# Performance work log

Measured on AMD Instinct MI355X. Metric: run time of the kernel, lower is better.

## Reference

```python
import jax, jax.numpy as jnp
import numpy as np

N, K = 8192, 133
N_LAYERS = 6
HID = 64
# mmpose RealNVP coupling masks: [0,1],[1,0] repeated 3 times
MASK = jnp.array([[0.0, 1.0], [1.0, 0.0]] * 3, dtype=jnp.float32)  # [6,2]


def _mlp(x, w1, b1, w2, b2, w3, b3):
    # x: [P,2] -> [P,2]; LeakyReLU slope 0.01 (torch default)
    h = jax.nn.leaky_relu(x @ w1.T + b1, 0.01)
    h = jax.nn.leaky_relu(h @ w2.T + b2, 0.01)
    return h @ w3.T + b3


def _flow_log_prob(x, s_w1, s_b1, s_w2, s_b2, s_w3, s_b3,
                   t_w1, t_b1, t_w2, t_b2, t_w3, t_b3):
    # RealNVP backward pass: x -> z, accumulating log-det Jacobian
    z = x
    log_det = jnp.zeros(x.shape[0], x.dtype)
    for i in reversed(range(N_LAYERS)):
        m = MASK[i]
        z_ = m * z
        s = jnp.tanh(_mlp(z_, s_w1[i], s_b1[i], s_w2[i], s_b2[i], s_w3[i], s_b3[i])) * (1.0 - m)
        t = _mlp(z_, t_w1[i], t_b1[i], t_w2[i], t_b2[i], t_w3[i], t_b3[i]) * (1.0 - m)
        z = (1.0 - m) * (z - t) * jnp.exp(-s) + z_
        log_det = log_det - s.sum(axis=1)
    # standard 2D normal prior log-prob
    prior_lp = -0.5 * jnp.sum(z * z, axis=1) - jnp.log(2.0 * jnp.pi)
    return prior_lp + log_det


def setup_inputs() -> dict:
    key = jax.random.key(0)
    ks = jax.random.split(key, 16)
    inp = {
        'pred': jax.random.normal(ks[0], (N, K, 4), dtype=jnp.float32),
        'target': jax.random.normal(ks[1], (N, K, 2), dtype=jnp.float32),
        'target_weight': jax.random.uniform(ks[2], (N, K), dtype=jnp.float32),
    }
    dims = [(HID, 2), (HID,), (HID, HID), (HID,), (2, HID), (2,)]
    names = ['w1', 'b1', 'w2', 'b2', 'w3', 'b3']
    kidx = 3
    for pfx in ('s', 't'):
        for nm, d in zip(names, dims):
            inp[f'{pfx}_{nm}'] = 0.1 * jax.random.normal(ks[kidx], (N_LAYERS,) + d, dtype=jnp.float32)
            kidx += 1
    return inp


def reference(pred, target, target_weight,
              s_w1, s_b1, s_w2, s_b2, s_w3, s_b3,
              t_w1, t_b1, t_w2, t_b2, t_w3, t_b3):
    miu = pred[:, :, :2]
    sigma = jnp.sqrt(jnp.abs(pred[:, :, 2:4]))  # sigmoid=False
    error = (miu - target) / (sigma + 1e-9)  # [N,K,2]
    log_phi = _flow_log_prob(error.reshape(-1, 2),
                             s_w1, s_b1, s_w2, s_b2, s_w3, s_b3,
                             t_w1, t_b1, t_w2, t_b2, t_w3, t_b3)
    log_phi = log_phi.reshape(pred.shape[0], pred.shape[1], 1)
    log_sigma = jnp.log(sigma)
    nf_loss = log_sigma - log_phi  # [N,K,2]
    # residual=True, q_distribution='laplace'
    loss_q = jnp.log(sigma * 2.0) + jnp.abs(error)
    loss = nf_loss + loss_q
    loss = loss * target_weight[:, :, None]  # use_target_weight=True
    loss = loss / pred.shape[0]  # size_average=True: divide by len(loss)=N
    return loss.sum()
```

## Files before the change

kernel.cpp:

```cpp
#include <hip/hip_runtime.h>

typedef _Float16 hfrag_t __attribute__((ext_vector_type(8)));
typedef _Float16 h2_t    __attribute__((ext_vector_type(2)));
typedef __attribute__((ext_vector_type(4))) float    f4_t;
typedef __attribute__((ext_vector_type(4))) unsigned u4_t;

#define LOG_2PI   1.8378770664093453f
#define TWO_LOG2  1.3862943611198906f
#define T_TILES   8
#define BLOCK     256
#define PTS_BLK   512
#define ZCLAMP    30000.0f

__device__ __forceinline__ unsigned pkh(float a, float b) {
  return __builtin_bit_cast(unsigned, __builtin_amdgcn_cvt_pkrtz(a, b));
}
__device__ __forceinline__ unsigned pk_fma_h(unsigned a, unsigned b, unsigned c) {
  unsigned d;
  asm("v_pk_fma_f16 %0, %1, %2, %3" : "=v"(d) : "v"(a), "v"(b), "v"(c));
  return d;
}
__device__ __forceinline__ unsigned pk_leaky_h(unsigned h, unsigned k01) {
  unsigned t, r;
  asm("v_pk_mul_f16 %0, %1, %2" : "=v"(t) : "v"(h), "v"(k01));
  asm("v_pk_max_f16 %0, %1, %2" : "=v"(r) : "v"(h), "v"(t));
  return r;
}
__device__ __forceinline__ float dot2h(unsigned a, unsigned b, float c) {
  return __builtin_amdgcn_fdot2(__builtin_bit_cast(h2_t, a), __builtin_bit_cast(h2_t, b), c, false);
}

__device__ __forceinline__ void stage_layer(u4_t* afr, const float* sW2, const float* tW2,
                                            int layer, int tid) {
  #pragma unroll
  for (int it = 0; it < 4; ++it) {
    int idx = tid + it * BLOCK;
    int l = idx & 63, f = (idx >> 6) & 7, m = (idx >> 9) & 1;
    int n = f & 3, q = f >> 2;
    int row = 16 * n + (l & 15), kb = 32 * q + 8 * (l >> 4);
    const float* src = (m ? tW2 : sW2) + layer * 4096 + row * 64 + kb;
    float4 a = *(const float4*)src;
    float4 b = *(const float4*)(src + 4);
    afr[(m * 8 + f) * 64 + l] =
        (u4_t){pkh(a.x, a.y), pkh(a.z, a.w), pkh(b.x, b.y), pkh(b.z, b.w)};
  }
}

__global__ __launch_bounds__(BLOCK)
void ihll_kernel(
    const float* __restrict__ pred, const float* __restrict__ targ, const float* __restrict__ twp,
    const float* __restrict__ sW1, const float* __restrict__ sB1, const float* __restrict__ sW2,
    const float* __restrict__ sB2, const float* __restrict__ sW3, const float* __restrict__ sB3,
    const float* __restrict__ tW1, const float* __restrict__ tB1, const float* __restrict__ tW2,
    const float* __restrict__ tB2, const float* __restrict__ tW3, const float* __restrict__ tB3,
    float* __restrict__ out, int M) {
  __shared__ u4_t     afr[2 * 8 * 64];
  __shared__ float4   zld[PTS_BLK];
  __shared__ float    pre0v[PTS_BLK];
  __shared__ unsigned c1h[6][2][32];
  __shared__ unsigned b1h[6][2][32];
  __shared__ unsigned w3h[6][2][4][8];
  __shared__ float    b2s[6][2][64];
  __shared__ float    wsum[4];

  const int tid  = threadIdx.x;
  const int lane = tid & 63, wave = tid >> 6;
  const int pr   = lane & 15, g = lane >> 4;
  const int pbase = blockIdx.x * PTS_BLK;
  const unsigned k01h = pkh(0.01f, 0.01f);

  for (int idx = tid; idx < 384; idx += BLOCK) {
    int i = idx >> 6, r = idx & 63, m = r >> 5, jp = r & 31;
    int jo = i & 1, jm = jo ^ 1;
    const float* w1 = m ? tW1 : sW1;  const float* b1 = m ? tB1 : sB1;
    c1h[i][m][jp] = pkh(w1[i * 128 + 4 * jp + jm], w1[i * 128 + 4 * jp + 2 + jm]);
    b1h[i][m][jp] = pkh(b1[i * 64 + 2 * jp], b1[i * 64 + 2 * jp + 1]);
  }
  for (int idx = tid; idx < 384; idx += BLOCK) {
    int i = idx >> 6, r = idx & 63, m = r >> 5, c = r & 31;
    int gg = c >> 3, c2 = c & 7, n = c2 >> 1, jj = c2 & 1;
    int jo = i & 1;
    const float* w3 = m ? tW3 : sW3;
    int row = 16 * n + 4 * gg + 2 * jj;
    w3h[i][m][gg][c2] = pkh(w3[i * 128 + jo * 64 + row], w3[i * 128 + jo * 64 + row + 1]);
  }
  for (int idx = tid; idx < 768; idx += BLOCK) {
    int i = idx >> 7, r = idx & 127, m = r >> 6, j = r & 63;
    const float* b2 = m ? tB2 : sB2;
    b2s[i][m][j] = b2[i * 64 + j];
  }
  #pragma unroll
  for (int it = 0; it < 2; ++it) {
    int idx = tid + it * BLOCK;
    int P = pbase + idx;
    float4 zs = make_float4(0.f, 0.f, 0.f, 0.f);
    if (P < M) {
      float4 p4 = ((const float4*)pred)[P];
      float2 t2 = ((const float2*)targ)[P];
      float s0 = sqrtf(fabsf(p4.z)), s1 = sqrtf(fabsf(p4.w));
      zs.x = (p4.x - t2.x) / (s0 + 1e-9f);
      zs.y = (p4.y - t2.y) / (s1 + 1e-9f);
    }
    zld[idx] = zs;
  }
  stage_layer(afr, sW2, tW2, 5, tid);
  __syncthreads();

  const int wbase = wave * (T_TILES * 16);
  const float* zldf = (const float*)zld;

  #pragma unroll 1
  for (int li = 0; li < 6; ++li) {
    const int i = 5 - li;
    const int jo = i & 1;
    const bool upd0 = (jo == 0);
    const float b3s = sB3[i * 2 + jo];
    const float b3t = tB3[i * 2 + jo];

    #pragma unroll
    for (int m = 0; m < 2; ++m) {
      u4_t af[8];
      #pragma unroll
      for (int f = 0; f < 8; ++f)
        af[f] = afr[(m * 8 + f) * 64 + lane];
      unsigned c1q[8], b1q[8];
      *(u4_t*)&c1q[0] = *(const u4_t*)&c1h[i][m][4 * g];
      *(u4_t*)&c1q[4] = *(const u4_t*)&c1h[i][m][16 + 4 * g];
      *(u4_t*)&b1q[0] = *(const u4_t*)&b1h[i][m][4 * g];
      *(u4_t*)&b1q[4] = *(const u4_t*)&b1h[i][m][16 + 4 * g];
      unsigned w3q[8];
      *(u4_t*)&w3q[0] = *(const u4_t*)&w3h[i][m][g][0];
      *(u4_t*)&w3q[4] = *(const u4_t*)&w3h[i][m][g][4];
      f4_t b2q[4];
      #pragma unroll
      for (int n = 0; n < 4; ++n)
        b2q[n] = *(const f4_t*)&b2s[i][m][n * 16 + 4 * g];

      #pragma unroll 1
      for (int t = 0; t < T_TILES; ++t) {
        const int widx = wbase + t * 16 + pr;
        float4 zv;
        float zin;
        if (m == 1) { zv = zld[widx]; zin = upd0 ? zv.y : zv.x; }
        else        { zin = zldf[4 * widx + (upd0 ? 1 : 0)]; }
        float zc = fmaxf(fminf(zin, ZCLAMP), -ZCLAMP);
        const unsigned zz = pkh(zc, zc);

        f4_t acc[4];
        #pragma unroll
        for (int q = 0; q < 2; ++q) {
          unsigned hh[4];
          #pragma unroll
          for (int e = 0; e < 4; ++e)
            hh[e] = pk_leaky_h(pk_fma_h(c1q[q * 4 + e], zz, b1q[q * 4 + e]), k01h);
          hfrag_t B = __builtin_bit_cast(hfrag_t, (u4_t){hh[0], hh[1], hh[2], hh[3]});
          #pragma unroll
          for (int n = 0; n < 4; ++n) {
            f4_t c = (q == 0) ? b2q[n] : acc[n];
            acc[n] = __builtin_amdgcn_mfma_f32_16x16x32_f16(
                __builtin_bit_cast(hfrag_t, af[q * 4 + n]), B, c, 0, 0, 0);
          }
        }
        float pa = 0.f;
        #pragma unroll
        for (int n = 0; n < 4; ++n) {
          unsigned x01 = pk_leaky_h(pkh(acc[n][0], acc[n][1]), k01h);
          unsigned x23 = pk_leaky_h(pkh(acc[n][2], acc[n][3]), k01h);
          pa = dot2h(x01, w3q[2 * n], pa);
          pa = dot2h(x23, w3q[2 * n + 1], pa);
        }
        pa += __shfl_xor(pa, 16);
        pa += __shfl_xor(pa, 32);

        if (m == 0) {
          if (g == 0) pre0v[widx] = pa;
        } else {
          float p0  = pre0v[widx];
          float sv  = 1.f - 2.f / (__expf(2.f * (p0 + b3s)) + 1.f);
          float tv  = pa + b3t;
          float zo  = upd0 ? zv.x : zv.y;
          float zn  = (zo - tv) * __expf(-sv);
          if (upd0) zv.x = zn; else zv.y = zn;
          zv.z -= sv;
          if (g == 0) zld[widx] = zv;
        }
      }
    }
    __syncthreads();
    if (li < 5) {
      stage_layer(afr, sW2, tW2, i - 1, tid);
      __syncthreads();
    }
  }

  float csum = 0.f;
  #pragma unroll
  for (int it = 0; it < 2; ++it) {
    int idx = tid + it * BLOCK;
    int P = pbase + idx;
    if (P < M) {
      float4 p4 = ((const float4*)pred)[P];
      float2 t2 = ((const float2*)targ)[P];
      float w   = twp[P];
      float s0 = sqrtf(fabsf(p4.z)), s1 = sqrtf(fabsf(p4.w));
      float e0 = (p4.x - t2.x) / (s0 + 1e-9f);
      float e1 = (p4.y - t2.y) / (s1 + 1e-9f);
      float bs = 2.f * (logf(s0) + logf(s1)) + TWO_LOG2 + fabsf(e0) + fabsf(e1);
      float4 zv = zld[idx];
      float prior = -0.5f * (zv.x * zv.x + zv.y * zv.y) - LOG_2PI;
      float lphi  = prior + zv.z;
      csum += (bs - 2.f * lphi) * w;
    }
  }
  #pragma unroll
  for (int off = 1; off <= 32; off <<= 1)
    csum += __shfl_xor(csum, off);
  if (lane == 0) wsum[wave] = csum;
  __syncthreads();
  if (tid == 0) {
    float tot = wsum[0] + wsum[1] + wsum[2] + wsum[3];
    atomicAdd(out, tot * (1.0f / 8192.0f));
  }
}

extern "C" void kernel_launch(void* const* d_in, const int* in_sizes, int n_in,
                              void* d_out, int out_size, void* d_ws, size_t ws_size,
                              hipStream_t stream) {
  const float* pred = (const float*)d_in[0];
  const float* targ = (const float*)d_in[1];
  const float* twp  = (const float*)d_in[2];
  const float* sW1 = (const float*)d_in[3];  const float* sB1 = (const float*)d_in[4];
  const float* sW2 = (const float*)d_in[5];  const float* sB2 = (const float*)d_in[6];
  const float* sW3 = (const float*)d_in[7];  const float* sB3 = (const float*)d_in[8];
  const float* tW1 = (const float*)d_in[9];  const float* tB1 = (const float*)d_in[10];
  const float* tW2 = (const float*)d_in[11]; const float* tB2 = (const float*)d_in[12];
  const float* tW3 = (const float*)d_in[13]; const float* tB3 = (const float*)d_in[14];

  const int M = in_sizes[2];
  const int blocks = (M + PTS_BLK - 1) / PTS_BLK;

  hipMemsetAsync(d_out, 0, sizeof(float), stream);
  hipLaunchKernelGGL(ihll_kernel, dim3(blocks), dim3(BLOCK), 0, stream,
                     pred, targ, twp, sW1, sB1, sW2, sB2, sW3, sB3,
                     tW1, tB1, tW2, tB2, tW3, tB3, (float*)d_out, M);
}
```

Before: 232.0 us.

## Process four point tiles per iteration to interleave MFMA chains

The inner tile loop now handles four 16-point tiles at once, giving four independent MFMA accumulator chains and four independent layer-1/epilogue streams so MFMA latency can be hidden by ILP. The s-network partial sums are reduced across lanes as packed fp16 pairs to cut shuffle count, and the kernel is hinted to run at 2 waves per EU. In exchange it raises register pressure and reduces the s-branch pre-activation sum to fp16 precision before the tanh.

```diff
diff --git a/kernel.cpp b/kernel.cpp
--- a/kernel.cpp
+++ b/kernel.cpp
@@ -18,6 +18,11 @@
 __device__ __forceinline__ unsigned pk_fma_h(unsigned a, unsigned b, unsigned c) {
   unsigned d;
   asm("v_pk_fma_f16 %0, %1, %2, %3" : "=v"(d) : "v"(a), "v"(b), "v"(c));
+  return d;
+}
+__device__ __forceinline__ unsigned pk_add_h(unsigned a, unsigned b) {
+  unsigned d;
+  asm("v_pk_add_f16 %0, %1, %2" : "=v"(d) : "v"(a), "v"(b));
   return d;
 }
 __device__ __forceinline__ unsigned pk_leaky_h(unsigned h, unsigned k01) {
@@ -47,6 +52,7 @@
 }
 
 __global__ __launch_bounds__(BLOCK)
+__attribute__((amdgpu_waves_per_eu(2)))
 void ihll_kernel(
     const float* __restrict__ pred, const float* __restrict__ targ, const float* __restrict__ twp,
     const float* __restrict__ sW1, const float* __restrict__ sB1, const float* __restrict__ sW2,
@@ -107,7 +113,6 @@
   __syncthreads();
 
   const int wbase = wave * (T_TILES * 16);
-  const float* zldf = (const float*)zld;
 
   #pragma unroll 1
   for (int li = 0; li < 6; ++li) {
@@ -137,52 +142,113 @@
         b2q[n] = *(const f4_t*)&b2s[i][m][n * 16 + 4 * g];
 
       #pragma unroll 1
-      for (int t = 0; t < T_TILES; ++t) {
-        const int widx = wbase + t * 16 + pr;
-        float4 zv;
-        float zin;
-        if (m == 1) { zv = zld[widx]; zin = upd0 ? zv.y : zv.x; }
-        else        { zin = zldf[4 * widx + (upd0 ? 1 : 0)]; }
-        float zc = fmaxf(fminf(zin, ZCLAMP), -ZCLAMP);
-        const unsigned zz = pkh(zc, zc);
-
-        f4_t acc[4];
+      for (int tt = 0; tt < T_TILES / 4; ++tt) {
+        const int w0 = wbase + (4 * tt) * 16 + pr;
+        float4 zv0 = zld[w0];
+        float4 zv1 = zld[w0 + 16];
+        float4 zv2 = zld[w0 + 32];
+        float4 zv3 = zld[w0 + 48];
+        float zi0 = upd0 ? zv0.y : zv0.x;
+        float zi1 = upd0 ? zv1.y : zv1.x;
+        float zi2 = upd0 ? zv2.y : zv2.x;
+        float zi3 = upd0 ? zv3.y : zv3.x;
+        zi0 = fmaxf(fminf(zi0, ZCLAMP), -ZCLAMP);
+        zi1 = fmaxf(fminf(zi1, ZCLAMP), -ZCLAMP);
+        zi2 = fmaxf(fminf(zi2, ZCLAMP), -ZCLAMP);
+        zi3 = fmaxf(fminf(zi3, ZCLAMP), -ZCLAMP);
+        const unsigned zz0 = pkh(zi0, zi0), zz1 = pkh(zi1, zi1);
+        const unsigned zz2 = pkh(zi2, zi2), zz3 = pkh(zi3, zi3);
+
+        f4_t acc0[4], acc1[4], acc2[4], acc3[4];
         #pragma unroll
         for (int q = 0; q < 2; ++q) {
-          unsigned hh[4];
+          unsigned h0[4], h1v[4], h2v[4], h3[4];
           #pragma unroll
-          for (int e = 0; e < 4; ++e)
-            hh[e] = pk_leaky_h(pk_fma_h(c1q[q * 4 + e], zz, b1q[q * 4 + e]), k01h);
-          hfrag_t B = __builtin_bit_cast(hfrag_t, (u4_t){hh[0], hh[1], hh[2], hh[3]});
+          for (int e = 0; e < 4; ++e) {
+            h0[e]  = pk_leaky_h(pk_fma_h(c1q[q * 4 + e], zz0, b1q[q * 4 + e]), k01h);
+            h1v[e] = pk_leaky_h(pk_fma_h(c1q[q * 4 + e], zz1, b1q[q * 4 + e]), k01h);
+            h2v[e] = pk_leaky_h(pk_fma_h(c1q[q * 4 + e], zz2, b1q[q * 4 + e]), k01h);
+            h3[e]  = pk_leaky_h(pk_fma_h(c1q[q * 4 + e], zz3, b1q[q * 4 + e]), k01h);
+          }
+          hfrag_t B0 = __builtin_bit_cast(hfrag_t, (u4_t){h0[0], h0[1], h0[2], h0[3]});
+          hfrag_t B1 = __builtin_bit_cast(hfrag_t, (u4_t){h1v[0], h1v[1], h1v[2], h1v[3]});
+          hfrag_t B2 = __builtin_bit_cast(hfrag_t, (u4_t){h2v[0], h2v[1], h2v[2], h2v[3]});
+          hfrag_t B3 = __builtin_bit_cast(hfrag_t, (u4_t){h3[0], h3[1], h3[2], h3[3]});
           #pragma unroll
           for (int n = 0; n < 4; ++n) {
-            f4_t c = (q == 0) ? b2q[n] : acc[n];
-            acc[n] = __builtin_amdgcn_mfma_f32_16x16x32_f16(
-                __builtin_bit_cast(hfrag_t, af[q * 4 + n]), B, c, 0, 0, 0);
+            hfrag_t A = __builtin_bit_cast(hfrag_t, af[q * 4 + n]);
+            acc0[n] = __builtin_amdgcn_mfma_f32_16x16x32_f16(A, B0, (q == 0) ? b2q[n] : acc0[n], 0, 0, 0);
+            acc1[n] = __builtin_amdgcn_mfma_f32_16x16x32_f16(A, B1, (q == 0) ? b2q[n] : acc1[n], 0, 0, 0);
+            acc2[n] = __builtin_amdgcn_mfma_f32_16x16x32_f16(A, B2, (q == 0) ? b2q[n] : acc2[n], 0, 0, 0);
+            acc3[n] = __builtin_amdgcn_mfma_f32_16x16x32_f16(A, B3, (q == 0) ? b2q[n] : acc3[n], 0, 0, 0);
           }
         }
-        float pa = 0.f;
+        float p0a = 0.f, p0b = 0.f, p1a = 0.f, p1b = 0.f;
+        float p2a = 0.f, p2b = 0.f, p3a = 0.f, p3b = 0.f;
         #pragma unroll
         for (int n = 0; n < 4; ++n) {
-          unsigned x01 = pk_leaky_h(pkh(acc[n][0], acc[n][1]), k01h);
-          unsigned x23 = pk_leaky_h(pkh(acc[n][2], acc[n][3]), k01h);
-          pa = dot2h(x01, w3q[2 * n], pa);
-          pa = dot2h(x23, w3q[2 * n + 1], pa);
+          unsigned a01 = pk_leaky_h(pkh(acc0[n][0], acc0[n][1]), k01h);
+          unsigned a23 = pk_leaky_h(pkh(acc0[n][2], acc0[n][3]), k01h);
+          unsigned b01 = pk_leaky_h(pkh(acc1[n][0], acc1[n][1]), k01h);
+          unsigned b23 = pk_leaky_h(pkh(acc1[n][2], acc1[n][3]), k01h);
+          unsigned c01 = pk_leaky_h(pkh(acc2[n][0], acc2[n][1]), k01h);
+          unsigned c23 = pk_leaky_h(pkh(acc2[n][2], acc2[n][3]), k01h);
+          unsigned d01 = pk_leaky_h(pkh(acc3[n][0], acc3[n][1]), k01h);
+          unsigned d23 = pk_leaky_h(pkh(acc3[n][2], acc3[n][3]), k01h);
+          if (n < 2) {
+            p0a = dot2h(a01, w3q[2 * n], p0a);  p0a = dot2h(a23, w3q[2 * n + 1], p0a);
+            p1a = dot2h(b01, w3q[2 * n], p1a);  p1a = dot2h(b23, w3q[2 * n + 1], p1a);
+            p2a = dot2h(c01, w3q[2 * n], p2a);  p2a = dot2h(c23, w3q[2 * n + 1], p2a);
+            p3a = dot2h(d01, w3q[2 * n], p3a);  p3a = dot2h(d23, w3q[2 * n + 1], p3a);
+          } else {
+            p0b = dot2h(a01, w3q[2 * n], p0b);  p0b = dot2h(a23, w3q[2 * n + 1], p0b);
+            p1b = dot2h(b01, w3q[2 * n], p1b);  p1b = dot2h(b23, w3q[2 * n + 1], p1b);
+            p2b = dot2h(c01, w3q[2 * n], p2b);  p2b = dot2h(c23, w3q[2 * n + 1], p2b);
+            p3b = dot2h(d01, w3q[2 * n], p3b);  p3b = dot2h(d23, w3q[2 * n + 1], p3b);
+          }
         }
-        pa += __shfl_xor(pa, 16);
-        pa += __shfl_xor(pa, 32);
+        float pt0 = p0a + p0b, pt1 = p1a + p1b, pt2 = p2a + p2b, pt3 = p3a + p3b;
 
         if (m == 0) {
-          if (g == 0) pre0v[widx] = pa;
+          unsigned r01 = pkh(pt0, pt1), r23 = pkh(pt2, pt3);
+          r01 = pk_add_h(r01, __shfl_xor(r01, 16));
+          r23 = pk_add_h(r23, __shfl_xor(r23, 16));
+          r01 = pk_add_h(r01, __shfl_xor(r01, 32));
+          r23 = pk_add_h(r23, __shfl_xor(r23, 32));
+          if (g == 0) {
+            h2_t v01 = __builtin_bit_cast(h2_t, r01);
+            h2_t v23 = __builtin_bit_cast(h2_t, r23);
+            pre0v[w0]      = (float)v01[0];
+            pre0v[w0 + 16] = (float)v01[1];
+            pre0v[w0 + 32] = (float)v23[0];
+            pre0v[w0 + 48] = (float)v23[1];
+          }
         } else {
-          float p0  = pre0v[widx];
-          float sv  = 1.f - 2.f / (__expf(2.f * (p0 + b3s)) + 1.f);
-          float tv  = pa + b3t;
-          float zo  = upd0 ? zv.x : zv.y;
-          float zn  = (zo - tv) * __expf(-sv);
-          if (upd0) zv.x = zn; else zv.y = zn;
-          zv.z -= sv;
-          if (g == 0) zld[widx] = zv;
+          pt0 += __shfl_xor(pt0, 16);  pt0 += __shfl_xor(pt0, 32);
+          pt1 += __shfl_xor(pt1, 16);  pt1 += __shfl_xor(pt1, 32);
+          pt2 += __shfl_xor(pt2, 16);  pt2 += __shfl_xor(pt2, 32);
+          pt3 += __shfl_xor(pt3, 16);  pt3 += __shfl_xor(pt3, 32);
+          float s0v = 1.f - 2.f / (__expf(2.f * (pre0v[w0]      + b3s)) + 1.f);
+          float s1v = 1.f - 2.f / (__expf(2.f * (pre0v[w0 + 16] + b3s)) + 1.f);
+          float s2v = 1.f - 2.f / (__expf(2.f * (pre0v[w0 + 32] + b3s)) + 1.f);
+          float s3v = 1.f - 2.f / (__expf(2.f * (pre0v[w0 + 48] + b3s)) + 1.f);
+          float zo0 = upd0 ? zv0.x : zv0.y;
+          float zo1 = upd0 ? zv1.x : zv1.y;
+          float zo2 = upd0 ? zv2.x : zv2.y;
+          float zo3 = upd0 ? zv3.x : zv3.y;
+          float zn0 = (zo0 - (pt0 + b3t)) * __expf(-s0v);
+          float zn1 = (zo1 - (pt1 + b3t)) * __expf(-s1v);
+          float zn2 = (zo2 - (pt2 + b3t)) * __expf(-s2v);
+          float zn3 = (zo3 - (pt3 + b3t)) * __expf(-s3v);
+          if (upd0) { zv0.x = zn0; zv1.x = zn1; zv2.x = zn2; zv3.x = zn3; }
+          else      { zv0.y = zn0; zv1.y = zn1; zv2.y = zn2; zv3.y = zn3; }
+          zv0.z -= s0v;  zv1.z -= s1v;  zv2.z -= s2v;  zv3.z -= s3v;
+          if (g == 0) {
+            zld[w0]      = zv0;
+            zld[w0 + 16] = zv1;
+            zld[w0 + 32] = zv2;
+            zld[w0 + 48] = zv3;
+          }
         }
       }
     }
```

After: 224.7 us, median of 2. 3.1% less time.

## Keep per-point flow state in registers and unroll tile loop with smaller blocks

Applied to the files above, without the earlier changes.

Each point's flow state (z0, z1, log-det and the s-branch pre-activation) now lives in per-thread registers instead of shared-memory arrays. This removes LDS reads and writes from every tile of every layer. The tile loop is fully unrolled, points per block are halved, and a waves-per-EU hint is added to trade register pressure for occupancy. Because all four lane groups now hold the same point, the epilogue counts each point four times. The final scale is divided by four more to compensate, and the log/sqrt epilogue work is repeated redundantly per lane group.

```diff
diff --git a/kernel.cpp b/kernel.cpp
--- a/kernel.cpp
+++ b/kernel.cpp
@@ -7,9 +7,9 @@
 
 #define LOG_2PI   1.8378770664093453f
 #define TWO_LOG2  1.3862943611198906f
-#define T_TILES   8
+#define T_TILES   4
 #define BLOCK     256
-#define PTS_BLK   512
+#define PTS_BLK   256
 #define ZCLAMP    30000.0f
 
 __device__ __forceinline__ unsigned pkh(float a, float b) {
@@ -47,6 +47,7 @@
 }
 
 __global__ __launch_bounds__(BLOCK)
+__attribute__((amdgpu_waves_per_eu(4)))
 void ihll_kernel(
     const float* __restrict__ pred, const float* __restrict__ targ, const float* __restrict__ twp,
     const float* __restrict__ sW1, const float* __restrict__ sB1, const float* __restrict__ sW2,
@@ -55,8 +56,6 @@
     const float* __restrict__ tB2, const float* __restrict__ tW3, const float* __restrict__ tB3,
     float* __restrict__ out, int M) {
   __shared__ u4_t     afr[2 * 8 * 64];
-  __shared__ float4   zld[PTS_BLK];
-  __shared__ float    pre0v[PTS_BLK];
   __shared__ unsigned c1h[6][2][32];
   __shared__ unsigned b1h[6][2][32];
   __shared__ unsigned w3h[6][2][4][8];
@@ -89,25 +88,23 @@
     const float* b2 = m ? tB2 : sB2;
     b2s[i][m][j] = b2[i * 64 + j];
   }
-  #pragma unroll
-  for (int it = 0; it < 2; ++it) {
-    int idx = tid + it * BLOCK;
-    int P = pbase + idx;
-    float4 zs = make_float4(0.f, 0.f, 0.f, 0.f);
+
+  float z0[T_TILES], z1[T_TILES], ld[T_TILES], pre0[T_TILES];
+  #pragma unroll
+  for (int t = 0; t < T_TILES; ++t) {
+    int P = pbase + wave * 64 + t * 16 + pr;
+    float e0 = 0.f, e1 = 0.f;
     if (P < M) {
       float4 p4 = ((const float4*)pred)[P];
       float2 t2 = ((const float2*)targ)[P];
       float s0 = sqrtf(fabsf(p4.z)), s1 = sqrtf(fabsf(p4.w));
-      zs.x = (p4.x - t2.x) / (s0 + 1e-9f);
-      zs.y = (p4.y - t2.y) / (s1 + 1e-9f);
-    }
-    zld[idx] = zs;
+      e0 = (p4.x - t2.x) / (s0 + 1e-9f);
+      e1 = (p4.y - t2.y) / (s1 + 1e-9f);
+    }
+    z0[t] = e0; z1[t] = e1; ld[t] = 0.f; pre0[t] = 0.f;
   }
   stage_layer(afr, sW2, tW2, 5, tid);
   __syncthreads();
-
-  const int wbase = wave * (T_TILES * 16);
-  const float* zldf = (const float*)zld;
 
   #pragma unroll 1
   for (int li = 0; li < 6; ++li) {
@@ -136,15 +133,11 @@
       for (int n = 0; n < 4; ++n)
         b2q[n] = *(const f4_t*)&b2s[i][m][n * 16 + 4 * g];
 
-      #pragma unroll 1
+      #pragma unroll
       for (int t = 0; t < T_TILES; ++t) {
-        const int widx = wbase + t * 16 + pr;
-        float4 zv;
-        float zin;
-        if (m == 1) { zv = zld[widx]; zin = upd0 ? zv.y : zv.x; }
-        else        { zin = zldf[4 * widx + (upd0 ? 1 : 0)]; }
-        float zc = fmaxf(fminf(zin, ZCLAMP), -ZCLAMP);
-        const unsigned zz = pkh(zc, zc);
+        float zin = upd0 ? z1[t] : z0[t];
+        zin = fmaxf(fminf(zin, ZCLAMP), -ZCLAMP);
+        const unsigned zz = pkh(zin, zin);
 
         f4_t acc[4];
         #pragma unroll
@@ -161,28 +154,32 @@
                 __builtin_bit_cast(hfrag_t, af[q * 4 + n]), B, c, 0, 0, 0);
           }
         }
-        float pa = 0.f;
+        float pa_ = 0.f, pb_ = 0.f;
         #pragma unroll
         for (int n = 0; n < 4; ++n) {
-          unsigned x01 = pk_leaky_h(pkh(acc[n][0], acc[n][1]), k01h);
-          unsigned x23 = pk_leaky_h(pkh(acc[n][2], acc[n][3]), k01h);
-          pa = dot2h(x01, w3q[2 * n], pa);
-          pa = dot2h(x23, w3q[2 * n + 1], pa);
+          unsigned a01 = pk_leaky_h(pkh(acc[n][0], acc[n][1]), k01h);
+          unsigned a23 = pk_leaky_h(pkh(acc[n][2], acc[n][3]), k01h);
+          if (n < 2) {
+            pa_ = dot2h(a01, w3q[2 * n], pa_);
+            pa_ = dot2h(a23, w3q[2 * n + 1], pa_);
+          } else {
+            pb_ = dot2h(a01, w3q[2 * n], pb_);
+            pb_ = dot2h(a23, w3q[2 * n + 1], pb_);
+          }
         }
-        pa += __shfl_xor(pa, 16);
-        pa += __shfl_xor(pa, 32);
+        float pt = pa_ + pb_;
+        pt += __shfl_xor(pt, 16);
+        pt += __shfl_xor(pt, 32);
 
         if (m == 0) {
-          if (g == 0) pre0v[widx] = pa;
+          pre0[t] = pt;
         } else {
-          float p0  = pre0v[widx];
-          float sv  = 1.f - 2.f / (__expf(2.f * (p0 + b3s)) + 1.f);
-          float tv  = pa + b3t;
-          float zo  = upd0 ? zv.x : zv.y;
-          float zn  = (zo - tv) * __expf(-sv);
-          if (upd0) zv.x = zn; else zv.y = zn;
-          zv.z -= sv;
-          if (g == 0) zld[widx] = zv;
+          float sv = 1.f - 2.f / (__expf(2.f * (pre0[t] + b3s)) + 1.f);
+          float tv = pt + b3t;
+          float zo = upd0 ? z0[t] : z1[t];
+          float zn = (zo - tv) * __expf(-sv);
+          if (upd0) z0[t] = zn; else z1[t] = zn;
+          ld[t] -= sv;
         }
       }
     }
@@ -195,9 +192,8 @@
 
   float csum = 0.f;
   #pragma unroll
-  for (int it = 0; it < 2; ++it) {
-    int idx = tid + it * BLOCK;
-    int P = pbase + idx;
+  for (int t = 0; t < T_TILES; ++t) {
+    int P = pbase + wave * 64 + t * 16 + pr;
     if (P < M) {
       float4 p4 = ((const float4*)pred)[P];
       float2 t2 = ((const float2*)targ)[P];
@@ -206,9 +202,8 @@
       float e0 = (p4.x - t2.x) / (s0 + 1e-9f);
       float e1 = (p4.y - t2.y) / (s1 + 1e-9f);
       float bs = 2.f * (logf(s0) + logf(s1)) + TWO_LOG2 + fabsf(e0) + fabsf(e1);
-      float4 zv = zld[idx];
-      float prior = -0.5f * (zv.x * zv.x + zv.y * zv.y) - LOG_2PI;
-      float lphi  = prior + zv.z;
+      float prior = -0.5f * (z0[t] * z0[t] + z1[t] * z1[t]) - LOG_2PI;
+      float lphi  = prior + ld[t];
       csum += (bs - 2.f * lphi) * w;
     }
   }
@@ -219,7 +214,7 @@
   __syncthreads();
   if (tid == 0) {
     float tot = wsum[0] + wsum[1] + wsum[2] + wsum[3];
-    atomicAdd(out, tot * (1.0f / 8192.0f));
+    atomicAdd(out, tot * (1.0f / 32768.0f));
   }
 }
 
```

Measured after the change: 228.4 us. No clear change (-1.5%).
